# Optimization experiments

Hardware: AMD Instinct MI355X
Metric: run time of the kernel (lower is better)

The kernel has to match this reference:

```python
import jax, jax.numpy as jnp
import numpy as np

B, IN_DIM, OUT_DIM, MV = 8192, 256, 256, 8


def setup_inputs() -> dict:
    key = jax.random.key(0)
    k1, k2 = jax.random.split(key)
    x = jax.random.normal(k1, (B, IN_DIM, MV), dtype=jnp.float32)
    weights = jax.random.normal(k2, (IN_DIM, OUT_DIM, MV), dtype=jnp.float32) * 0.01
    bias = jnp.zeros((OUT_DIM, MV), dtype=jnp.float32)
    return {"x": x, "weights": weights, "bias": bias}


def reference(x, weights, bias):
    # Simplified GA-3D geometric product, summed over in_dim (j), per out_dim (i):
    #   y[..., i, 0] = sum_j x[..., j, 0]*W[j,i,0] + x[..., j, 1]*W[j,i,1] + x[..., j, 2]*W[j,i,2]
    #   y[..., i, 4] = sum_j x[..., j, 1]*W[j,i,2] - x[..., j, 2]*W[j,i,1] + x[..., j, 4]*W[j,i,0]
    #   all other multivector components receive only the bias.
    # Scalar component: dot over first 3 multivector slots.
    c0 = jnp.einsum('bjk,jik->bi', x[..., 0:3], weights[..., 0:3])  # (B, OUT_DIM)
    # Bivector component e23: x1*w2 - x2*w1 + x4*w0.
    xv = jnp.stack([x[..., 1], -x[..., 2], x[..., 4]], axis=-1)          # (B, IN_DIM, 3)
    wv = jnp.stack([weights[..., 2], weights[..., 1], weights[..., 0]], axis=-1)  # (IN_DIM, OUT_DIM, 3)
    c4 = jnp.einsum('bjk,jik->bi', xv, wv)  # (B, OUT_DIM)
    y = jnp.broadcast_to(bias, (x.shape[0],) + bias.shape)  # (B, OUT_DIM, MV)
    y = y.at[..., 0].add(c0).at[..., 4].add(c4)
    return y
```

## Files before the change

kernel.cpp:

```cpp
#include <hip/hip_runtime.h>
#include <hip/hip_bf16.h>

typedef __attribute__((ext_vector_type(4))) float f32x4;
typedef __attribute__((ext_vector_type(8))) short bf16x8;

#define CS 516

__device__ __forceinline__ short f2bf(float f) {
  __hip_bfloat16 h = __float2bfloat16(f);
  return __builtin_bit_cast(short, h);
}

#define GLD_LDS16(gp, lp)                                                    \
  __builtin_amdgcn_global_load_lds(                                          \
      (const __attribute__((address_space(1))) unsigned int*)(gp),           \
      (__attribute__((address_space(3))) unsigned int*)(lp), 16, 0, 0)

__global__ __launch_bounds__(256) void ga_prep_B(const float* __restrict__ W,
                                                 short* __restrict__ Bp) {
  const int gid = blockIdx.x * 256 + threadIdx.x;
  const int l  = gid & 63;
  const int cg = (gid >> 6) & 31;
  const int it = gid >> 11;
  const int ln = l & 15, q = l >> 4;
  const int hc = cg >> 4;
  const int i  = (cg & 15) * 16 + ln;
  const int j0 = it * 8 + q * 2;
  const float4* W4 = (const float4*)W;

  bf16x8 o;
#pragma unroll
  for (int jj = 0; jj < 2; ++jj) {
    const float4 wv = W4[((j0 + jj) * 256 + i) * 2];
    if (!hc) {
      o[jj * 4 + 0] = f2bf(wv.x); o[jj * 4 + 1] = f2bf(wv.y);
      o[jj * 4 + 2] = f2bf(wv.z); o[jj * 4 + 3] = 0;
    } else {
      o[jj * 4 + 0] = 0;           o[jj * 4 + 1] = f2bf(wv.z);
      o[jj * 4 + 2] = f2bf(-wv.y); o[jj * 4 + 3] = f2bf(wv.x);
    }
  }
  *(bf16x8*)&Bp[(size_t)gid * 8] = o;
}

__global__ __launch_bounds__(256) void ga_prep_A(const float* __restrict__ x,
                                                 short* __restrict__ A) {
  const int g = blockIdx.x * 256 + threadIdx.x;
  const int row = g >> 7, rem = g & 127;
  const int q = rem >> 5, c = rem & 31;
  const int cp = c ^ ((row & 7) << 2);
  const float4* x4 = (const float4*)x + (size_t)(row * 256 + q * 64 + c * 2) * 2;
  const float4 a0 = x4[0], a1 = x4[1], b0 = x4[2], b1 = x4[3];
  bf16x8 o;
  o[0] = f2bf(a0.x); o[1] = f2bf(a0.y); o[2] = f2bf(a0.z); o[3] = f2bf(a1.x);
  o[4] = f2bf(b0.x); o[5] = f2bf(b0.y); o[6] = f2bf(b0.z); o[7] = f2bf(b1.x);
  *(bf16x8*)&A[((size_t)row * 128 + q * 32 + cp) * 8] = o;
}

__global__ __launch_bounds__(1024, 4) void ga_mv_main(
    const short* __restrict__ A, const short* __restrict__ Bp,
    const float* __restrict__ bias, float* __restrict__ y) {
  __shared__ __align__(16) char smem[65536];
  short* lds_s = (short*)smem;
  float* c_lds = (float*)smem;

  const int t = threadIdx.x;
  const int bm = blockIdx.x;
  const int lane = t & 63, w = t >> 6;
  const int ln = lane & 15, qq = lane >> 4, lnl = lane & 7;
  const int R0 = bm * 32;

  const short* asrc = A + ((size_t)(R0 + (t >> 5)) * 128 + (t & 31)) * 8;
#pragma unroll
  for (int q = 0; q < 4; ++q)
    GLD_LDS16(asrc + q * 256, lds_s + q * 8192 + t * 8);

  const size_t bbase = (size_t)w * 1024 + lane * 8;
  bf16x8 Bf[4][2];
#define LB(itv, b)                                                           \
  {                                                                          \
    const short* p = Bp + (size_t)(itv) * 16384 + bbase;                     \
    Bf[b][0] = *(const bf16x8*)(p);                                          \
    Bf[b][1] = *(const bf16x8*)(p + 512);                                    \
  }
  LB(0, 0);
  LB(1, 1);
  LB(2, 2);
  LB(3, 3);

  __syncthreads();

  f32x4 acc[2][2] = {};
  const int abase = ln * 256 + qq * 8;
#pragma unroll
  for (int it = 0; it < 32; ++it) {
    const int q = it >> 3, tau = it & 7;
    const short* Aq = lds_s + q * 8192 + abase + ((tau ^ lnl) << 5);
    const bf16x8 af0 = *(const bf16x8*)Aq;
    const bf16x8 af1 = *(const bf16x8*)(Aq + 4096);
#pragma unroll
    for (int n = 0; n < 2; ++n) {
      acc[0][n] = __builtin_amdgcn_mfma_f32_16x16x32_bf16(af0, Bf[it & 3][n],
                                                          acc[0][n], 0, 0, 0);
      acc[1][n] = __builtin_amdgcn_mfma_f32_16x16x32_bf16(af1, Bf[it & 3][n],
                                                          acc[1][n], 0, 0, 0);
    }
    if (it + 4 < 32) LB(it + 4, it & 3);
  }
  __syncthreads();

  const int h = t & 1, p = (t >> 1) & 255, rh = t >> 9;
  const float4 bv = ((const float4*)bias)[p * 2 + h];
  f32x4* y4 = (f32x4*)y;

#pragma unroll
  for (int ep = 0; ep < 2; ++ep) {
    if (ep) __syncthreads();
#pragma unroll
    for (int n = 0; n < 2; ++n)
#pragma unroll
      for (int r = 0; r < 4; ++r)
        c_lds[(qq * 4 + r) * CS + w * 32 + n * 16 + ln] = acc[ep][n][r];
    __syncthreads();
#pragma unroll
    for (int rr = 0; rr < 8; ++rr) {
      const int row = rr * 2 + rh;
      f32x4 o;
      o[0] = bv.x; o[1] = bv.y; o[2] = bv.z; o[3] = bv.w;
      o[0] += c_lds[row * CS + h * 256 + p];
      __builtin_nontemporal_store(
          o, &y4[((size_t)(R0 + ep * 16 + row) * 256 + p) * 2 + h]);
    }
  }
}

extern "C" void kernel_launch(void* const* d_in, const int* in_sizes, int n_in,
                              void* d_out, int out_size, void* d_ws, size_t ws_size,
                              hipStream_t stream) {
  const float* x = (const float*)d_in[0];
  const float* W = (const float*)d_in[1];
  const float* bias = (const float*)d_in[2];
  float* y = (float*)d_out;
  short* Bp = (short*)d_ws;
  short* A = (short*)d_ws + (1 << 19);

  ga_prep_B<<<dim3(256), dim3(256), 0, stream>>>(W, Bp);
  ga_prep_A<<<dim3(4096), dim3(256), 0, stream>>>(x, A);
  ga_mv_main<<<dim3(256), dim3(1024), 0, stream>>>(A, Bp, bias, y);
}
```

Measured before the change: 133.4 us.

## Derive bivector weight fragment in-register from scalar fragment, halving B traffic

The prep kernel now writes only the scalar-component weight fragments (w0,w1,w2,0). The main kernel builds the bivector fragment (0,w2,-w1,w0) from them with bit shifts and a sign flip in registers. This halves the packed B buffer and the per-iteration global loads in the main loop, at the cost of a few integer ops per iteration. The regular __syncthreads calls are also replaced by a custom barrier that waits only on LDS counters, and the C staging layout is rearranged to match.

```diff
diff --git a/kernel.cpp b/kernel.cpp
--- a/kernel.cpp
+++ b/kernel.cpp
@@ -2,6 +2,7 @@
 #include <hip/hip_bf16.h>
 
 typedef __attribute__((ext_vector_type(4))) float f32x4;
+typedef __attribute__((ext_vector_type(4))) unsigned int u32x4;
 typedef __attribute__((ext_vector_type(8))) short bf16x8;
 
 #define CS 516
@@ -16,15 +17,22 @@
       (const __attribute__((address_space(1))) unsigned int*)(gp),           \
       (__attribute__((address_space(3))) unsigned int*)(lp), 16, 0, 0)
 
+#define QBAR()                                              \
+  {                                                         \
+    asm volatile("s_waitcnt lgkmcnt(0)" ::: "memory");      \
+    __builtin_amdgcn_sched_barrier(0);                      \
+    __builtin_amdgcn_s_barrier();                           \
+    __builtin_amdgcn_sched_barrier(0);                      \
+  }
+
 __global__ __launch_bounds__(256) void ga_prep_B(const float* __restrict__ W,
                                                  short* __restrict__ Bp) {
   const int gid = blockIdx.x * 256 + threadIdx.x;
   const int l  = gid & 63;
-  const int cg = (gid >> 6) & 31;
-  const int it = gid >> 11;
+  const int cg = (gid >> 6) & 15;
+  const int it = gid >> 10;
   const int ln = l & 15, q = l >> 4;
-  const int hc = cg >> 4;
-  const int i  = (cg & 15) * 16 + ln;
+  const int i  = cg * 16 + ln;
   const int j0 = it * 8 + q * 2;
   const float4* W4 = (const float4*)W;
 
@@ -32,13 +40,8 @@
 #pragma unroll
   for (int jj = 0; jj < 2; ++jj) {
     const float4 wv = W4[((j0 + jj) * 256 + i) * 2];
-    if (!hc) {
-      o[jj * 4 + 0] = f2bf(wv.x); o[jj * 4 + 1] = f2bf(wv.y);
-      o[jj * 4 + 2] = f2bf(wv.z); o[jj * 4 + 3] = 0;
-    } else {
-      o[jj * 4 + 0] = 0;           o[jj * 4 + 1] = f2bf(wv.z);
-      o[jj * 4 + 2] = f2bf(-wv.y); o[jj * 4 + 3] = f2bf(wv.x);
-    }
+    o[jj * 4 + 0] = f2bf(wv.x); o[jj * 4 + 1] = f2bf(wv.y);
+    o[jj * 4 + 2] = f2bf(wv.z); o[jj * 4 + 3] = 0;
   }
   *(bf16x8*)&Bp[(size_t)gid * 8] = o;
 }
@@ -75,14 +78,9 @@
   for (int q = 0; q < 4; ++q)
     GLD_LDS16(asrc + q * 256, lds_s + q * 8192 + t * 8);
 
-  const size_t bbase = (size_t)w * 1024 + lane * 8;
-  bf16x8 Bf[4][2];
-#define LB(itv, b)                                                           \
-  {                                                                          \
-    const short* p = Bp + (size_t)(itv) * 16384 + bbase;                     \
-    Bf[b][0] = *(const bf16x8*)(p);                                          \
-    Bf[b][1] = *(const bf16x8*)(p + 512);                                    \
-  }
+  const size_t bbase = (size_t)w * 512 + lane * 8;
+  bf16x8 Bf[4];
+#define LB(itv, b) { Bf[b] = *(const bf16x8*)(Bp + (size_t)(itv) * 8192 + bbase); }
   LB(0, 0);
   LB(1, 1);
   LB(2, 2);
@@ -98,16 +96,21 @@
     const short* Aq = lds_s + q * 8192 + abase + ((tau ^ lnl) << 5);
     const bf16x8 af0 = *(const bf16x8*)Aq;
     const bf16x8 af1 = *(const bf16x8*)(Aq + 4096);
-#pragma unroll
-    for (int n = 0; n < 2; ++n) {
-      acc[0][n] = __builtin_amdgcn_mfma_f32_16x16x32_bf16(af0, Bf[it & 3][n],
-                                                          acc[0][n], 0, 0, 0);
-      acc[1][n] = __builtin_amdgcn_mfma_f32_16x16x32_bf16(af1, Bf[it & 3][n],
-                                                          acc[1][n], 0, 0, 0);
-    }
+    const bf16x8 F = Bf[it & 3];
+    const u32x4 fu = __builtin_bit_cast(u32x4, F);
+    u32x4 gu;
+    gu.x = fu.y << 16;
+    gu.y = ((fu.x >> 16) | (fu.x << 16)) ^ 0x8000u;
+    gu.z = fu.w << 16;
+    gu.w = ((fu.z >> 16) | (fu.z << 16)) ^ 0x8000u;
+    const bf16x8 G = __builtin_bit_cast(bf16x8, gu);
+    acc[0][0] = __builtin_amdgcn_mfma_f32_16x16x32_bf16(af0, F, acc[0][0], 0, 0, 0);
+    acc[1][0] = __builtin_amdgcn_mfma_f32_16x16x32_bf16(af1, F, acc[1][0], 0, 0, 0);
+    acc[0][1] = __builtin_amdgcn_mfma_f32_16x16x32_bf16(af0, G, acc[0][1], 0, 0, 0);
+    acc[1][1] = __builtin_amdgcn_mfma_f32_16x16x32_bf16(af1, G, acc[1][1], 0, 0, 0);
     if (it + 4 < 32) LB(it + 4, it & 3);
   }
-  __syncthreads();
+  QBAR();
 
   const int h = t & 1, p = (t >> 1) & 255, rh = t >> 9;
   const float4 bv = ((const float4*)bias)[p * 2 + h];
@@ -115,13 +118,13 @@
 
 #pragma unroll
   for (int ep = 0; ep < 2; ++ep) {
-    if (ep) __syncthreads();
+    if (ep) QBAR();
 #pragma unroll
     for (int n = 0; n < 2; ++n)
 #pragma unroll
       for (int r = 0; r < 4; ++r)
-        c_lds[(qq * 4 + r) * CS + w * 32 + n * 16 + ln] = acc[ep][n][r];
-    __syncthreads();
+        c_lds[(qq * 4 + r) * CS + n * 256 + w * 16 + ln] = acc[ep][n][r];
+    QBAR();
 #pragma unroll
     for (int rr = 0; rr < 8; ++rr) {
       const int row = rr * 2 + rh;
@@ -142,9 +145,9 @@
   const float* bias = (const float*)d_in[2];
   float* y = (float*)d_out;
   short* Bp = (short*)d_ws;
-  short* A = (short*)d_ws + (1 << 19);
+  short* A = (short*)d_ws + (1 << 18);
 
-  ga_prep_B<<<dim3(256), dim3(256), 0, stream>>>(W, Bp);
+  ga_prep_B<<<dim3(128), dim3(256), 0, stream>>>(W, Bp);
   ga_prep_A<<<dim3(4096), dim3(256), 0, stream>>>(x, A);
   ga_mv_main<<<dim3(256), dim3(1024), 0, stream>>>(A, Bp, bias, y);
 }
```

Measured after the change: 128.8 us. 3.4% less time.
